# Kernel optimization log

Hardware: AMD Instinct MI355X
Metric: run time of the kernel (lower is better)

The kernel has to match this reference:

```python
import jax, jax.numpy as jnp
import numpy as np

NHEAD = 16


def setup_inputs() -> dict:
    key = jax.random.key(0)
    ks = jax.random.split(key, 6)
    S, B, D = 2048, 2, 1024
    std = float(np.sqrt(6.0 / (D + D)))  # xavier_uniform bound
    inp = {
        "query": jax.random.normal(ks[0], (S, B, D), jnp.float32),
        "key": jax.random.normal(ks[1], (S, B, D), jnp.float32),
        "value": jax.random.normal(ks[2], (S, B, D), jnp.float32),
        "Wq": jax.random.uniform(ks[3], (D, D), jnp.float32, -std, std),
        "bq": jnp.ones((D,), jnp.float32),
        "Wk": jax.random.uniform(ks[4], (D, D), jnp.float32, -std, std),
        "bk": jnp.ones((D,), jnp.float32),
        "Wv": jax.random.uniform(ks[5], (D, D), jnp.float32, -std, std),
        "bv": jnp.ones((D,), jnp.float32),
    }
    return inp


def reference(query, key, value, Wq, bq, Wk, bk, Wv, bv):
    S, B, D = query.shape
    h = NHEAD
    d = D // h
    scale = jnp.asarray(d ** 0.5, query.dtype)
    # projections (nn.Linear: x @ W^T + b)
    q = (query @ Wq.T + bq).reshape(S, B, h, d)
    k = (key @ Wk.T + bk).reshape(S, B, h, d)
    v = (value @ Wv.T + bv).reshape(S, B, h, d)
    # batch_first=False path: scores [b,h,i,j], softmax over j, then AV
    scores = jnp.einsum('ibhd,jbhd->bhij', q, k) / scale
    attn = jax.nn.softmax(scores, axis=-1)
    out = jnp.einsum('bhij,jbhd->ibhd', attn, v).reshape(S, B, D)
    return out
```

## Files before the change

kernel.cpp:

```cpp
#include <hip/hip_runtime.h>
#include <hip/hip_bf16.h>

#define S_LEN 2048
#define BATCH 2
#define DMODEL 1024
#define NHEAD 16
#define HDIM 64
#define MTOT (S_LEN * BATCH)
#define QKV_ELEMS ((size_t)MTOT * DMODEL)
#define XOFF (3 * QKV_ELEMS)
#define WOFF (XOFF + 3 * QKV_ELEMS)
#define WSEG ((size_t)DMODEL * DMODEL)

typedef __bf16 bf16x8 __attribute__((ext_vector_type(8)));
typedef unsigned short u16x8 __attribute__((ext_vector_type(8)));
typedef float f32x4 __attribute__((ext_vector_type(4)));
typedef unsigned int u32x4 __attribute__((ext_vector_type(4)));

__device__ __forceinline__ unsigned short f2bf(float f) {
    unsigned int u = __float_as_uint(f);
    u += 0x7FFFu + ((u >> 16) & 1u);
    return (unsigned short)(u >> 16);
}

__device__ __forceinline__ unsigned int pack2(float lo, float hi) {
    __hip_bfloat162 h = __float22bfloat162_rn(make_float2(lo, hi));
    unsigned int r;
    __builtin_memcpy(&r, &h, 4);
    return r;
}

__device__ __forceinline__ void gload_lds16(const void* g, void* l) {
    __builtin_amdgcn_global_load_lds(
        (const __attribute__((address_space(1))) unsigned int*)g,
        (__attribute__((address_space(3))) unsigned int*)l, 16, 0, 0);
}

__global__ __launch_bounds__(256) void cvt_kernel(
        const float* __restrict__ Xq, const float* __restrict__ Xk,
        const float* __restrict__ Xv, const float* __restrict__ Wq,
        const float* __restrict__ Wk, const float* __restrict__ Wv,
        unsigned short* __restrict__ ws)
{
    const int seg = blockIdx.y;
    const float* src;
    unsigned short* dst;
    int n4;
    if (seg < 3) {
        src = (seg == 0) ? Xq : (seg == 1) ? Xk : Xv;
        dst = ws + XOFF + (size_t)seg * QKV_ELEMS;
        n4  = (int)(QKV_ELEMS / 4);
    } else {
        const int s = seg - 3;
        src = (s == 0) ? Wq : (s == 1) ? Wk : Wv;
        dst = ws + WOFF + (size_t)s * WSEG;
        n4  = (int)(WSEG / 4);
    }
    const int stride = gridDim.x * blockDim.x;
    for (int i = blockIdx.x * blockDim.x + threadIdx.x; i < n4; i += stride) {
        const float4 v = ((const float4*)src)[i];
        uint2 o;
        o.x = pack2(v.x, v.y);
        o.y = pack2(v.z, v.w);
        ((uint2*)dst)[i] = o;
    }
}

#define PBM 128
#define PBN 128
#define PBK 32
#define QSCALE 0.18033688011112042f

__global__ __launch_bounds__(256, 3) void proj_kernel(
        const unsigned short* __restrict__ wsin,
        const float* __restrict__ bq, const float* __restrict__ bk,
        const float* __restrict__ bv, unsigned short* __restrict__ wsout)
{
    const int work = (blockIdx.x & 7) * 96 + (blockIdx.x >> 3);
    const int t    = work >> 8;
    const int rem  = work & 255;
    const int m0   = (rem >> 3) * PBM;
    const int n0   = (rem & 7) * PBN;

    const unsigned short* X = wsin + XOFF + (size_t)t * QKV_ELEMS;
    const unsigned short* W = wsin + WOFF + (size_t)t * WSEG;
    const float* bias = (t == 0) ? bq : (t == 1) ? bk : bv;
    unsigned short* out = wsout + (size_t)t * QKV_ELEMS;
    const float scale = (t == 0) ? QSCALE : 1.0f;

    __shared__ __align__(16) unsigned short Abuf[2][PBM * PBK];
    __shared__ __align__(16) unsigned short Bbuf[2][PBN * PBK];

    const int tid  = threadIdx.x;
    const int wave = tid >> 6;
    const int lane = tid & 63;
    const int lrow = lane & 15;
    const int lg   = lane >> 4;
    const int wr = (wave >> 1) * 64;
    const int wc = (wave & 1) * 64;

    f32x4 acc[4][4];
#pragma unroll
    for (int i = 0; i < 4; ++i)
#pragma unroll
        for (int j = 0; j < 4; ++j)
            acc[i][j] = (f32x4){0.f, 0.f, 0.f, 0.f};

    const int srow_ = tid >> 2;
    const int sc_   = tid & 3;
    const int gsw = (lg ^ (lrow & 3)) * 8;

#pragma unroll
    for (int i0 = 0; i0 < 2; ++i0) {
        const int row = i0 * 64 + srow_;
        const int c   = sc_ ^ (row & 3);
        gload_lds16(X + (size_t)(m0 + row) * DMODEL + c * 8, &Abuf[0][i0 * 2048 + tid * 8]);
        gload_lds16(W + (size_t)(n0 + row) * DMODEL + c * 8, &Bbuf[0][i0 * 2048 + tid * 8]);
    }
    __syncthreads();

    int cur = 0;
    for (int k0 = 0; k0 < DMODEL; k0 += PBK) {
        if (k0 + PBK < DMODEL) {
#pragma unroll
            for (int i0 = 0; i0 < 2; ++i0) {
                const int row = i0 * 64 + srow_;
                const int c   = sc_ ^ (row & 3);
                gload_lds16(X + (size_t)(m0 + row) * DMODEL + k0 + PBK + c * 8,
                            &Abuf[cur ^ 1][i0 * 2048 + tid * 8]);
                gload_lds16(W + (size_t)(n0 + row) * DMODEL + k0 + PBK + c * 8,
                            &Bbuf[cur ^ 1][i0 * 2048 + tid * 8]);
            }
        }

        bf16x8 af[4], bw[4];
#pragma unroll
        for (int i = 0; i < 4; ++i) {
            af[i] = *(const bf16x8*)&Abuf[cur][(wr + i * 16 + lrow) * PBK + gsw];
            bw[i] = *(const bf16x8*)&Bbuf[cur][(wc + i * 16 + lrow) * PBK + gsw];
        }
        __builtin_amdgcn_s_setprio(1);
#pragma unroll
        for (int i = 0; i < 4; ++i)
#pragma unroll
            for (int j = 0; j < 4; ++j)
                acc[i][j] = __builtin_amdgcn_mfma_f32_16x16x32_bf16(af[i], bw[j], acc[i][j], 0, 0, 0);
        __builtin_amdgcn_s_setprio(0);

        __syncthreads();
        cur ^= 1;
    }

#pragma unroll
    for (int j = 0; j < 4; ++j) {
        const int n  = n0 + wc + j * 16 + lrow;
        const float bv_ = bias[n];
        const int h  = n >> 6;
        const int dd = n & 63;
#pragma unroll
        for (int i = 0; i < 4; ++i) {
#pragma unroll
            for (int r = 0; r < 4; ++r) {
                const int m = m0 + wr + i * 16 + lg * 4 + r;
                const int s = m >> 1;
                const int b = m & 1;
                const float v = (acc[i][j][r] + bv_) * scale;
                size_t idx;
                if (t == 2)
                    idx = ((size_t)((b * NHEAD + h) * HDIM + dd)) * S_LEN + s;
                else
                    idx = ((size_t)((b * NHEAD + h) * S_LEN + s)) * HDIM + dd;
                out[idx] = f2bf(v);
            }
        }
    }
}

#define NT (S_LEN / 64)
#define PUSTR 17

__global__ __launch_bounds__(512, 4) void attn_kernel(
        const unsigned short* __restrict__ ws, float* __restrict__ out)
{
    const unsigned short* Qw = ws;
    const unsigned short* Kw = ws + QKV_ELEMS;
    const unsigned short* Vw = ws + 2 * QKV_ELEMS;

    const int bid = blockIdx.x;
    const int idx = bid >> 3;
    const int bh  = (bid & 7) * 4 + (idx >> 4);
    const int q0  = (idx & 15) * 128;

    __shared__ __align__(16) unsigned short Kbuf[2][64 * 64];
    __shared__ __align__(16) unsigned short Vbuf[2][64 * 64];
    __shared__ unsigned int Pu[8][32 * PUSTR];

    const int tid  = threadIdx.x;
    const int wave = tid >> 6;
    const int lane = tid & 63;
    const int lrow = lane & 15;
    const int lg   = lane >> 4;

    const size_t base = (size_t)bh * S_LEN * HDIM;
    const int qrow = q0 + wave * 16 + lrow;

    bf16x8 qf[2];
#pragma unroll
    for (int c = 0; c < 2; ++c)
        qf[c] = *(const bf16x8*)(Qw + base + (size_t)qrow * HDIM + c * 32 + lg * 8);

    bf16x8 ones;
    {
        u16x8 o;
#pragma unroll
        for (int e = 0; e < 8; ++e) o[e] = 0x3F80;
        ones = __builtin_bit_cast(bf16x8, o);
    }

    f32x4 O[4], Lacc;
#pragma unroll
    for (int dt = 0; dt < 4; ++dt) O[dt] = (f32x4){0.f, 0.f, 0.f, 0.f};
    Lacc = (f32x4){0.f, 0.f, 0.f, 0.f};
    float mrun = -__builtin_inff();

    const int srow = tid >> 3;
    const int sgrp = (tid & 7) ^ (srow & 7);
    const int dsto = tid * 8;

    gload_lds16(Kw + base + (size_t)srow * HDIM + sgrp * 8,  &Kbuf[0][dsto]);
    gload_lds16(Vw + base + (size_t)srow * S_LEN + sgrp * 8, &Vbuf[0][dsto]);
    __syncthreads();

    int cur = 0;
    for (int t = 0; t < NT; ++t) {
        if (t + 1 < NT) {
            const int sn = (t + 1) * 64;
            gload_lds16(Kw + base + (size_t)(sn + srow) * HDIM + sgrp * 8, &Kbuf[cur ^ 1][dsto]);
            gload_lds16(Vw + base + (size_t)srow * S_LEN + sn + sgrp * 8, &Vbuf[cur ^ 1][dsto]);
        }

        const unsigned short* Klds = Kbuf[cur];
        const unsigned short* Vlds = Vbuf[cur];

        f32x4 S[4];
#pragma unroll
        for (int kt = 0; kt < 4; ++kt) S[kt] = (f32x4){0.f, 0.f, 0.f, 0.f};
        __builtin_amdgcn_s_setprio(1);
#pragma unroll
        for (int kt = 0; kt < 4; ++kt) {
#pragma unroll
            for (int c = 0; c < 2; ++c) {
                const int g = ((c * 4 + lg) ^ (lrow & 7)) * 8;
                const bf16x8 ka = *(const bf16x8*)&Klds[(kt * 16 + lrow) * 64 + g];
                S[kt] = __builtin_amdgcn_mfma_f32_16x16x32_bf16(ka, qf[c], S[kt], 0, 0, 0);
            }
        }
        __builtin_amdgcn_s_setprio(0);

        float m0_ = fmaxf(fmaxf(S[0][0], S[0][1]), fmaxf(S[0][2], S[0][3]));
        float m1_ = fmaxf(fmaxf(S[1][0], S[1][1]), fmaxf(S[1][2], S[1][3]));
        float m2_ = fmaxf(fmaxf(S[2][0], S[2][1]), fmaxf(S[2][2], S[2][3]));
        float m3_ = fmaxf(fmaxf(S[3][0], S[3][1]), fmaxf(S[3][2], S[3][3]));
        float mx = fmaxf(fmaxf(m0_, m1_), fmaxf(m2_, m3_));
        mx = fmaxf(mx, __shfl_xor(mx, 16, 64));
        mx = fmaxf(mx, __shfl_xor(mx, 32, 64));

        if (!__all(mx - mrun <= 8.0f)) {
            const float mnew = fmaxf(mrun, mx);
            const float ex   = exp2f(mrun - mnew);
            mrun = mnew;
#pragma unroll
            for (int dt = 0; dt < 4; ++dt) O[dt] *= ex;
            Lacc *= ex;
        }

#pragma unroll
        for (int kt = 0; kt < 4; ++kt)
#pragma unroll
            for (int r = 0; r < 4; ++r)
                S[kt][r] = exp2f(S[kt][r] - mrun);

#pragma unroll
        for (int kt = 0; kt < 4; ++kt) {
#pragma unroll
            for (int i = 0; i < 2; ++i) {
                const unsigned int dw = pack2(S[kt][2 * i], S[kt][2 * i + 1]);
                const int kp = kt * 8 + lg * 2 + i;
                Pu[wave][kp * PUSTR + lrow] = dw;
            }
        }
        __asm__ volatile("" ::: "memory");

        __builtin_amdgcn_s_setprio(1);
        bf16x8 pb[2];
#pragma unroll
        for (int c = 0; c < 2; ++c) {
            u32x4 pu;
#pragma unroll
            for (int e = 0; e < 4; ++e)
                pu[e] = Pu[wave][(c * 16 + lg * 4 + e) * PUSTR + lrow];
            pb[c] = __builtin_bit_cast(bf16x8, pu);
        }
#pragma unroll
        for (int dt = 0; dt < 4; ++dt) {
#pragma unroll
            for (int c = 0; c < 2; ++c) {
                const int g = ((c * 4 + lg) ^ (lrow & 7)) * 8;
                const bf16x8 va = *(const bf16x8*)&Vlds[(dt * 16 + lrow) * 64 + g];
                O[dt] = __builtin_amdgcn_mfma_f32_16x16x32_bf16(va, pb[c], O[dt], 0, 0, 0);
            }
        }
        Lacc = __builtin_amdgcn_mfma_f32_16x16x32_bf16(ones, pb[0], Lacc, 0, 0, 0);
        Lacc = __builtin_amdgcn_mfma_f32_16x16x32_bf16(ones, pb[1], Lacc, 0, 0, 0);
        __builtin_amdgcn_s_setprio(0);

        __syncthreads();
        cur ^= 1;
    }

    const int bb = bh >> 4;
    const int hh = bh & 15;
    const float inv = 1.0f / Lacc[0];
    float* op = out + (size_t)qrow * (BATCH * DMODEL) + bb * DMODEL + hh * HDIM;
#pragma unroll
    for (int dt = 0; dt < 4; ++dt) {
        float4 v;
        v.x = O[dt][0] * inv; v.y = O[dt][1] * inv;
        v.z = O[dt][2] * inv; v.w = O[dt][3] * inv;
        *(float4*)(op + dt * 16 + lg * 4) = v;
    }
}

extern "C" void kernel_launch(void* const* d_in, const int* in_sizes, int n_in,
                              void* d_out, int out_size, void* d_ws, size_t ws_size,
                              hipStream_t stream) {
    const float* q  = (const float*)d_in[0];
    const float* k  = (const float*)d_in[1];
    const float* v  = (const float*)d_in[2];
    const float* Wq = (const float*)d_in[3];
    const float* bq = (const float*)d_in[4];
    const float* Wk = (const float*)d_in[5];
    const float* bk = (const float*)d_in[6];
    const float* Wv = (const float*)d_in[7];
    const float* bv = (const float*)d_in[8];
    unsigned short* ws = (unsigned short*)d_ws;
    float* out = (float*)d_out;

    cvt_kernel<<<dim3(1024, 6), dim3(256), 0, stream>>>(q, k, v, Wq, Wk, Wv, ws);
    proj_kernel<<<dim3(768), dim3(256), 0, stream>>>(ws, bq, bk, bv, ws);
    attn_kernel<<<dim3(512), dim3(512), 0, stream>>>(ws, out);
}
```

Measured before the change: 138.1 us.

## Rework attention to 32x32 MFMA with split-KV wave pairs and merge

The attention kernel moves from 16x16x32 to 32x32x16 bf16 MFMA tiles, so each wave covers 32 query rows. The two waves of a pair each take alternate 32-key tiles and merge their softmax states through shared memory at the end. The launch changes to 1024 blocks of 256 threads, with a four-slot K/V ring and a new LDS swizzle. The goal is fewer LDS reads per MFMA and better occupancy, at the cost of a final cross-wave merge and more registers per wave.

```diff
diff --git a/kernel.cpp b/kernel.cpp
--- a/kernel.cpp
+++ b/kernel.cpp
@@ -15,6 +15,7 @@
 typedef __bf16 bf16x8 __attribute__((ext_vector_type(8)));
 typedef unsigned short u16x8 __attribute__((ext_vector_type(8)));
 typedef float f32x4 __attribute__((ext_vector_type(4)));
+typedef float f32x16 __attribute__((ext_vector_type(16)));
 typedef unsigned int u32x4 __attribute__((ext_vector_type(4)));
 
 __device__ __forceinline__ unsigned short f2bf(float f) {
@@ -176,10 +177,9 @@
     }
 }
 
-#define NT (S_LEN / 64)
-#define PUSTR 17
-
-__global__ __launch_bounds__(512, 4) void attn_kernel(
+#define NP 32
+
+__global__ __launch_bounds__(256, 4) void attn_kernel(
         const unsigned short* __restrict__ ws, float* __restrict__ out)
 {
     const unsigned short* Qw = ws;
@@ -188,26 +188,29 @@
 
     const int bid = blockIdx.x;
     const int idx = bid >> 3;
-    const int bh  = (bid & 7) * 4 + (idx >> 4);
-    const int q0  = (idx & 15) * 128;
-
-    __shared__ __align__(16) unsigned short Kbuf[2][64 * 64];
-    __shared__ __align__(16) unsigned short Vbuf[2][64 * 64];
-    __shared__ unsigned int Pu[8][32 * PUSTR];
+    const int bh  = (bid & 7) * 4 + (idx >> 5);
+    const int q0  = (idx & 31) * 64;
+
+    __shared__ __align__(16) unsigned short SMEM[20480];
+    unsigned short* Kb = SMEM;
+    unsigned short* Vb = SMEM + 8192;
+    unsigned int*   Pb = (unsigned int*)(SMEM + 16384);
 
     const int tid  = threadIdx.x;
     const int wave = tid >> 6;
     const int lane = tid & 63;
-    const int lrow = lane & 15;
-    const int lg   = lane >> 4;
+    const int l31  = lane & 31;
+    const int half = lane >> 5;
+    const int qsub = wave >> 1;
+    const int pw   = wave & 1;
 
     const size_t base = (size_t)bh * S_LEN * HDIM;
-    const int qrow = q0 + wave * 16 + lrow;
-
-    bf16x8 qf[2];
-#pragma unroll
-    for (int c = 0; c < 2; ++c)
-        qf[c] = *(const bf16x8*)(Qw + base + (size_t)qrow * HDIM + c * 32 + lg * 8);
+    const int qrow = q0 + qsub * 32 + l31;
+
+    bf16x8 qf[4];
+#pragma unroll
+    for (int c = 0; c < 4; ++c)
+        qf[c] = *(const bf16x8*)(Qw + base + (size_t)qrow * HDIM + c * 16 + half * 8);
 
     bf16x8 ones;
     {
@@ -217,117 +220,141 @@
         ones = __builtin_bit_cast(bf16x8, o);
     }
 
-    f32x4 O[4], Lacc;
-#pragma unroll
-    for (int dt = 0; dt < 4; ++dt) O[dt] = (f32x4){0.f, 0.f, 0.f, 0.f};
-    Lacc = (f32x4){0.f, 0.f, 0.f, 0.f};
+    f32x16 Od0, Od1, Lacc;
+#pragma unroll
+    for (int i = 0; i < 16; ++i) { Od0[i] = 0.f; Od1[i] = 0.f; Lacc[i] = 0.f; }
     float mrun = -__builtin_inff();
 
-    const int srow = tid >> 3;
-    const int sgrp = (tid & 7) ^ (srow & 7);
-    const int dsto = tid * 8;
-
-    gload_lds16(Kw + base + (size_t)srow * HDIM + sgrp * 8,  &Kbuf[0][dsto]);
-    gload_lds16(Vw + base + (size_t)srow * S_LEN + sgrp * 8, &Vbuf[0][dsto]);
+    unsigned int* PuW = Pb + wave * 512;
+
+    const int ksrow = tid >> 3;
+    const int ksg   = (tid & 7) ^ (ksrow & 7);
+    const int vrow  = tid >> 2;
+    const int vsg   = (tid & 3) ^ ((vrow >> 1) & 3);
+
+    int gk[4], gv[2];
+#pragma unroll
+    for (int c = 0; c < 4; ++c) gk[c] = ((c * 2 + half) ^ (l31 & 7)) * 8;
+#pragma unroll
+    for (int c = 0; c < 2; ++c) gv[c] = ((c * 2 + half) ^ ((l31 >> 1) & 3)) * 8;
+
+#pragma unroll
+    for (int t0 = 0; t0 < 2; ++t0) {
+        gload_lds16(Kw + base + (size_t)(t0 * 32 + ksrow) * HDIM + ksg * 8, &Kb[t0 * 2048 + tid * 8]);
+        gload_lds16(Vw + base + (size_t)vrow * S_LEN + t0 * 32 + vsg * 8,   &Vb[t0 * 2048 + tid * 8]);
+    }
     __syncthreads();
 
-    int cur = 0;
-    for (int t = 0; t < NT; ++t) {
-        if (t + 1 < NT) {
-            const int sn = (t + 1) * 64;
-            gload_lds16(Kw + base + (size_t)(sn + srow) * HDIM + sgrp * 8, &Kbuf[cur ^ 1][dsto]);
-            gload_lds16(Vw + base + (size_t)srow * S_LEN + sn + sgrp * 8, &Vbuf[cur ^ 1][dsto]);
-        }
-
-        const unsigned short* Klds = Kbuf[cur];
-        const unsigned short* Vlds = Vbuf[cur];
-
-        f32x4 S[4];
-#pragma unroll
-        for (int kt = 0; kt < 4; ++kt) S[kt] = (f32x4){0.f, 0.f, 0.f, 0.f};
+    for (int p = 0; p < NP; ++p) {
+        if (p < NP - 1) {
+#pragma unroll
+            for (int u = 0; u < 2; ++u) {
+                const int tt = 2 * p + 2 + u;
+                gload_lds16(Kw + base + (size_t)(tt * 32 + ksrow) * HDIM + ksg * 8, &Kb[(tt & 3) * 2048 + tid * 8]);
+                gload_lds16(Vw + base + (size_t)vrow * S_LEN + tt * 32 + vsg * 8,   &Vb[(tt & 3) * 2048 + tid * 8]);
+            }
+        }
+
+        const int tm = 2 * p + pw;
+        const unsigned short* Klds = &Kb[(tm & 3) * 2048];
+        const unsigned short* Vlds = &Vb[(tm & 3) * 2048];
+
+        f32x16 S;
+#pragma unroll
+        for (int i = 0; i < 16; ++i) S[i] = 0.f;
         __builtin_amdgcn_s_setprio(1);
 #pragma unroll
-        for (int kt = 0; kt < 4; ++kt) {
-#pragma unroll
-            for (int c = 0; c < 2; ++c) {
-                const int g = ((c * 4 + lg) ^ (lrow & 7)) * 8;
-                const bf16x8 ka = *(const bf16x8*)&Klds[(kt * 16 + lrow) * 64 + g];
-                S[kt] = __builtin_amdgcn_mfma_f32_16x16x32_bf16(ka, qf[c], S[kt], 0, 0, 0);
-            }
+        for (int c = 0; c < 4; ++c) {
+            const bf16x8 ka = *(const bf16x8*)&Klds[l31 * 64 + gk[c]];
+            S = __builtin_amdgcn_mfma_f32_32x32x16_bf16(ka, qf[c], S, 0, 0, 0);
         }
         __builtin_amdgcn_s_setprio(0);
 
-        float m0_ = fmaxf(fmaxf(S[0][0], S[0][1]), fmaxf(S[0][2], S[0][3]));
-        float m1_ = fmaxf(fmaxf(S[1][0], S[1][1]), fmaxf(S[1][2], S[1][3]));
-        float m2_ = fmaxf(fmaxf(S[2][0], S[2][1]), fmaxf(S[2][2], S[2][3]));
-        float m3_ = fmaxf(fmaxf(S[3][0], S[3][1]), fmaxf(S[3][2], S[3][3]));
-        float mx = fmaxf(fmaxf(m0_, m1_), fmaxf(m2_, m3_));
-        mx = fmaxf(mx, __shfl_xor(mx, 16, 64));
+        float m8[8], m4[4];
+#pragma unroll
+        for (int i = 0; i < 8; ++i) m8[i] = fmaxf(S[i], S[i + 8]);
+#pragma unroll
+        for (int i = 0; i < 4; ++i) m4[i] = fmaxf(m8[i], m8[i + 4]);
+        float mx = fmaxf(fmaxf(m4[0], m4[1]), fmaxf(m4[2], m4[3]));
         mx = fmaxf(mx, __shfl_xor(mx, 32, 64));
 
         if (!__all(mx - mrun <= 8.0f)) {
             const float mnew = fmaxf(mrun, mx);
             const float ex   = exp2f(mrun - mnew);
             mrun = mnew;
-#pragma unroll
-            for (int dt = 0; dt < 4; ++dt) O[dt] *= ex;
+            Od0 *= ex;
+            Od1 *= ex;
             Lacc *= ex;
         }
 
 #pragma unroll
-        for (int kt = 0; kt < 4; ++kt)
-#pragma unroll
-            for (int r = 0; r < 4; ++r)
-                S[kt][r] = exp2f(S[kt][r] - mrun);
-
-#pragma unroll
-        for (int kt = 0; kt < 4; ++kt) {
-#pragma unroll
-            for (int i = 0; i < 2; ++i) {
-                const unsigned int dw = pack2(S[kt][2 * i], S[kt][2 * i + 1]);
-                const int kp = kt * 8 + lg * 2 + i;
-                Pu[wave][kp * PUSTR + lrow] = dw;
-            }
+        for (int i = 0; i < 16; ++i) S[i] = exp2f(S[i] - mrun);
+
+#pragma unroll
+        for (int w = 0; w < 8; ++w) {
+            const unsigned int pk = pack2(S[2 * w], S[2 * w + 1]);
+            const int kp = (w & 1) + 4 * (w >> 1) + 2 * half;
+            PuW[kp * 32 + l31] = pk;
         }
         __asm__ volatile("" ::: "memory");
 
         __builtin_amdgcn_s_setprio(1);
-        bf16x8 pb[2];
 #pragma unroll
         for (int c = 0; c < 2; ++c) {
             u32x4 pu;
 #pragma unroll
             for (int e = 0; e < 4; ++e)
-                pu[e] = Pu[wave][(c * 16 + lg * 4 + e) * PUSTR + lrow];
-            pb[c] = __builtin_bit_cast(bf16x8, pu);
-        }
-#pragma unroll
-        for (int dt = 0; dt < 4; ++dt) {
-#pragma unroll
-            for (int c = 0; c < 2; ++c) {
-                const int g = ((c * 4 + lg) ^ (lrow & 7)) * 8;
-                const bf16x8 va = *(const bf16x8*)&Vlds[(dt * 16 + lrow) * 64 + g];
-                O[dt] = __builtin_amdgcn_mfma_f32_16x16x32_bf16(va, pb[c], O[dt], 0, 0, 0);
-            }
-        }
-        Lacc = __builtin_amdgcn_mfma_f32_16x16x32_bf16(ones, pb[0], Lacc, 0, 0, 0);
-        Lacc = __builtin_amdgcn_mfma_f32_16x16x32_bf16(ones, pb[1], Lacc, 0, 0, 0);
+                pu[e] = PuW[(c * 8 + half * 4 + e) * 32 + l31];
+            const bf16x8 pb = __builtin_bit_cast(bf16x8, pu);
+            const bf16x8 va0 = *(const bf16x8*)&Vlds[l31 * 32 + gv[c]];
+            const bf16x8 va1 = *(const bf16x8*)&Vlds[(32 + l31) * 32 + gv[c]];
+            Od0  = __builtin_amdgcn_mfma_f32_32x32x16_bf16(va0,  pb, Od0,  0, 0, 0);
+            Od1  = __builtin_amdgcn_mfma_f32_32x32x16_bf16(va1,  pb, Od1,  0, 0, 0);
+            Lacc = __builtin_amdgcn_mfma_f32_32x32x16_bf16(ones, pb, Lacc, 0, 0, 0);
+        }
         __builtin_amdgcn_s_setprio(0);
 
         __syncthreads();
-        cur ^= 1;
-    }
-
-    const int bb = bh >> 4;
-    const int hh = bh & 15;
-    const float inv = 1.0f / Lacc[0];
-    float* op = out + (size_t)qrow * (BATCH * DMODEL) + bb * DMODEL + hh * HDIM;
-#pragma unroll
-    for (int dt = 0; dt < 4; ++dt) {
-        float4 v;
-        v.x = O[dt][0] * inv; v.y = O[dt][1] * inv;
-        v.z = O[dt][2] * inv; v.w = O[dt][3] * inv;
-        *(float4*)(op + dt * 16 + lg * 4) = v;
+    }
+
+    float* mrg = (float*)SMEM;
+    float* reg = mrg + qsub * 2176;
+    if (pw) {
+        reg[lane]      = mrun;
+        reg[64 + lane] = Lacc[0];
+#pragma unroll
+        for (int i = 0; i < 16; ++i) {
+            reg[128 + i * 64 + lane]        = Od0[i];
+            reg[128 + (16 + i) * 64 + lane] = Od1[i];
+        }
+    }
+    __syncthreads();
+    if (!pw) {
+        const float mb = reg[lane];
+        const float lb = reg[64 + lane];
+        const float ms = fmaxf(mrun, mb);
+        const float sa = exp2f(mrun - ms);
+        const float sb = exp2f(mb - ms);
+        const float linv = 1.0f / (Lacc[0] * sa + lb * sb);
+
+        const int bb = bh >> 4;
+        const int hh = bh & 15;
+        float* op = out + (size_t)qrow * (BATCH * DMODEL) + bb * DMODEL + hh * HDIM;
+#pragma unroll
+        for (int gg = 0; gg < 4; ++gg) {
+            const int d0 = gg * 8 + half * 4;
+            float4 v0, v1;
+            v0.x = (Od0[gg * 4 + 0] * sa + reg[128 + (gg * 4 + 0) * 64 + lane] * sb) * linv;
+            v0.y = (Od0[gg * 4 + 1] * sa + reg[128 + (gg * 4 + 1) * 64 + lane] * sb) * linv;
+            v0.z = (Od0[gg * 4 + 2] * sa + reg[128 + (gg * 4 + 2) * 64 + lane] * sb) * linv;
+            v0.w = (Od0[gg * 4 + 3] * sa + reg[128 + (gg * 4 + 3) * 64 + lane] * sb) * linv;
+            v1.x = (Od1[gg * 4 + 0] * sa + reg[128 + (16 + gg * 4 + 0) * 64 + lane] * sb) * linv;
+            v1.y = (Od1[gg * 4 + 1] * sa + reg[128 + (16 + gg * 4 + 1) * 64 + lane] * sb) * linv;
+            v1.z = (Od1[gg * 4 + 2] * sa + reg[128 + (16 + gg * 4 + 2) * 64 + lane] * sb) * linv;
+            v1.w = (Od1[gg * 4 + 3] * sa + reg[128 + (16 + gg * 4 + 3) * 64 + lane] * sb) * linv;
+            *(float4*)(op + d0)      = v0;
+            *(float4*)(op + 32 + d0) = v1;
+        }
     }
 }
 
@@ -348,5 +375,5 @@
 
     cvt_kernel<<<dim3(1024, 6), dim3(256), 0, stream>>>(q, k, v, Wq, Wk, Wv, ws);
     proj_kernel<<<dim3(768), dim3(256), 0, stream>>>(ws, bq, bk, bv, ws);
-    attn_kernel<<<dim3(512), dim3(512), 0, stream>>>(ws, out);
-}
+    attn_kernel<<<dim3(1024), dim3(256), 0, stream>>>(ws, out);
+}
```

Result: slower. 141.1 us (+2.2%).
